# Performance work log

Measured on AMD Instinct MI355X. Metric: run time of the kernel, lower is better.

Reference implementation:

```python
import jax, jax.numpy as jnp
import numpy as np

EMBED_DIM = 1024
N_HEADS = 16
HEAD_SIZE = EMBED_DIM // N_HEADS
SCALE = HEAD_SIZE ** -0.5


def setup_inputs() -> dict:
    key = jax.random.key(0)
    ks = jax.random.split(key, 11)
    B, Tq, Tk, C = 4, 1024, 1024, EMBED_DIM
    std = 0.02
    return {
        "q": jax.random.normal(ks[0], (B, Tq, C), jnp.float32),
        "k": jax.random.normal(ks[1], (B, Tk, C), jnp.float32),
        "v": jax.random.normal(ks[2], (B, Tk, C), jnp.float32),
        "Wq": jax.random.normal(ks[3], (C, C), jnp.float32) * std,
        "bq": jnp.zeros((C,), jnp.float32),
        "Wk": jax.random.normal(ks[4], (C, C), jnp.float32) * std,
        "bk": jnp.zeros((C,), jnp.float32),
        "Wv": jax.random.normal(ks[5], (C, C), jnp.float32) * std,
        "bv": jnp.zeros((C,), jnp.float32),
        "Wo": jax.random.normal(ks[6], (C, C), jnp.float32) * std,
        "bo": jnp.zeros((C,), jnp.float32),
    }


def reference(q, k, v, Wq, bq, Wk, bk, Wv, bv, Wo, bo):
    b, t, c = q.shape
    # linear projections (torch Linear: x @ W.T + b)
    qp = q @ Wq.T + bq            # [b, tq, c]
    kp = k @ Wk.T + bk            # [b, tk, c]
    vp = v @ Wv.T + bv            # [b, tk, c]
    # split heads: [b, h, t, d]
    qh = qp.reshape(b, t, N_HEADS, HEAD_SIZE).transpose(0, 2, 1, 3)
    kh = kp.reshape(b, kp.shape[1], N_HEADS, HEAD_SIZE).transpose(0, 2, 1, 3)
    vh = vp.reshape(b, vp.shape[1], N_HEADS, HEAD_SIZE).transpose(0, 2, 1, 3)
    # scaled dot-product attention
    scores = jnp.einsum('bhqd,bhkd->bhqk', qh, kh) * SCALE
    weights = jax.nn.softmax(scores, axis=-1)
    attn = jnp.einsum('bhqk,bhkd->bhqd', weights, vh)
    attn = attn.transpose(0, 2, 1, 3).reshape(b, t, c)
    out = attn @ Wo.T + bo
    return out
```

## Files before the change

kernel.cpp:

```cpp
#include <hip/hip_runtime.h>
#include <stdint.h>

typedef unsigned short u16;
typedef unsigned int   u32;
typedef __bf16 bf16;
typedef bf16  bf16x2 __attribute__((ext_vector_type(2)));
typedef bf16  bf16x8 __attribute__((ext_vector_type(8)));
typedef float f32x4  __attribute__((ext_vector_type(4)));

#define AS1 __attribute__((address_space(1)))
#define AS3 __attribute__((address_space(3)))


__device__ __forceinline__ u32 pk2(float lo, float hi) {
  bf16x2 t;
  t[0] = (bf16)lo;
  t[1] = (bf16)hi;
  return __builtin_bit_cast(u32, t);
}

__device__ __forceinline__ u16 b1(float f) {
  bf16 t = (bf16)f;
  return __builtin_bit_cast(u16, t);
}

__device__ __forceinline__ void gload_lds16(const void* src, void* dst) {
  __builtin_amdgcn_global_load_lds((const AS1 void*)src, (AS3 void*)dst, 16, 0, 0);
}

__device__ __forceinline__ bf16x8 fragS(const char* lds, int row, int kbyte) {
  return *(const bf16x8*)(lds + row * 128 + (kbyte ^ ((row & 7) << 4)));
}


__global__ __launch_bounds__(256) void cvt_w(
    const float* wq, const float* wk, const float* wv, const float* wo,
    u16* wqb, u16* wkb, u16* wvb, u16* wob)
{
  const float* src; u16* dst;
  switch (blockIdx.y) {
    case 0: src = wq; dst = wqb; break;
    case 1: src = wk; dst = wkb; break;
    case 2: src = wv; dst = wvb; break;
    default: src = wo; dst = wob; break;
  }
  const int n4 = 262144;
  int stride = gridDim.x * blockDim.x;
  for (int i = blockIdx.x * blockDim.x + threadIdx.x; i < n4; i += stride) {
    float4 f = ((const float4*)src)[i];
    uint2 o;
    o.x = pk2(f.x, f.y);
    o.y = pk2(f.z, f.w);
    ((uint2*)dst)[i] = o;
  }
}


template<int NC>
__device__ __forceinline__ void stageSw(const u16* gtile, char* lds, int tid)
{
  int w = tid >> 6, lane = tid & 63;
  int rr = lane >> 3;
  int cb = (lane & 7) << 4;
  #pragma unroll
  for (int i = 0; i < NC; ++i) {
    int c = i * 4 + w;
    int r = c * 8 + rr;
    gload_lds16((const char*)(gtile + r * 1024) + (cb ^ (rr << 4)), lds + c * 1024);
  }
}

__device__ __forceinline__ void loadA64(const float* gA, int tid,
                                        float4* pa, float4* pb)
{
  int r0 = tid >> 3, c8 = (tid & 7) << 3;
  #pragma unroll
  for (int i = 0; i < 2; ++i) {
    const float* p = gA + (i * 32 + r0) * 1024 + c8;
    pa[i] = *(const float4*)p;
    pb[i] = *(const float4*)(p + 4);
  }
}

__device__ __forceinline__ void writeA64(char* lds, int tid,
                                         const float4* pa, const float4* pb)
{
  int r0 = tid >> 3, cb = (tid & 7) << 4;
  #pragma unroll
  for (int i = 0; i < 2; ++i) {
    int r = i * 32 + r0;
    uint4 o;
    o.x = pk2(pa[i].x, pa[i].y);
    o.y = pk2(pa[i].z, pa[i].w);
    o.z = pk2(pb[i].x, pb[i].y);
    o.w = pk2(pb[i].z, pb[i].w);
    *(uint4*)(lds + r * 128 + (cb ^ ((r & 7) << 4))) = o;
  }
}

__device__ __forceinline__ void mfma_64x128(const char* As, const char* Bs,
                                            f32x4 acc[2][4], int lane,
                                            int wr, int wc)
{
  int g = lane >> 4;
  #pragma unroll
  for (int ks = 0; ks < 2; ++ks) {
    int kb = ks * 64 + (g << 4);
    bf16x8 af[2], bfr[4];
    #pragma unroll
    for (int m = 0; m < 2; ++m) af[m]  = fragS(As, wr * 32 + m * 16 + (lane & 15), kb);
    #pragma unroll
    for (int n = 0; n < 4; ++n) bfr[n] = fragS(Bs, wc * 64 + n * 16 + (lane & 15), kb);
    #pragma unroll
    for (int m = 0; m < 2; ++m)
      #pragma unroll
      for (int n = 0; n < 4; ++n)
        acc[m][n] = __builtin_amdgcn_mfma_f32_16x16x32_bf16(af[m], bfr[n], acc[m][n], 0, 0, 0);
  }
}


__global__ __launch_bounds__(256, 4) void proj_gemm(
    const float* qf, const float* kf, const float* vf,
    const u16* wqb, const u16* wkb, const u16* wvb,
    const float* bq, const float* bk, const float* bv,
    u16* qh, u16* kh, u16* vt)
{
  __shared__ alignas(16) char As[8192];
  __shared__ alignas(16) char Bs[16384];
  int tid = threadIdx.x;
  int bi = blockIdx.x & 63, bj = blockIdx.x >> 6;
  int z = blockIdx.z;
  const float* A = (z == 0) ? qf : (z == 1) ? kf : vf;
  const u16* W = (z == 0) ? wqb : (z == 1) ? wkb : wvb;
  const float* bias = (z == 0) ? bq : (z == 1) ? bk : bv;
  u16* dst = (z == 0) ? qh : (z == 1) ? kh : vt;

  int lane = tid & 63;
  int wr = (tid >> 7) & 1, wc = (tid >> 6) & 1;

  float4 pa[2], pb[2];
  loadA64(A + bi * 65536, tid, pa, pb);

  f32x4 acc[2][4] = {};
  for (int kt = 0; kt < 16; ++kt) {
    writeA64(As, tid, pa, pb);
    stageSw<4>(W + bj * 131072 + kt * 64, Bs, tid);
    if (kt < 15)
      loadA64(A + bi * 65536 + (kt + 1) * 64, tid, pa, pb);
    __syncthreads();
    mfma_64x128(As, Bs, acc, lane, wr, wc);
    __syncthreads();
  }

  int rbase = bi * 64 + wr * 32 + ((lane >> 4) << 2);
  int cbase = bj * 128 + wc * 64;
  #pragma unroll
  for (int n = 0; n < 4; ++n) {
    int col = cbase + n * 16 + (lane & 15);
    float bsv = bias[col];
    int h = col >> 6, d = col & 63;
    #pragma unroll
    for (int m = 0; m < 2; ++m) {
      #pragma unroll
      for (int r = 0; r < 4; ++r) {
        int R = rbase + m * 16 + r;
        int b = R >> 10, t = R & 1023;
        u16 val = b1(acc[m][n][r] + bsv);
        if (z < 2) dst[(((b * 16 + h) * 1024 + t) << 6) + d] = val;
        else       dst[(((b * 16 + h) * 64 + d) << 10) + t] = val;
      }
    }
  }
}


__global__ __launch_bounds__(256, 4) void out_gemm(
    const u16* attn, const u16* wob, const float* bo, float* out)
{
  __shared__ alignas(16) char As[8192];
  __shared__ alignas(16) char Bs[16384];
  int tid = threadIdx.x;
  int bi = blockIdx.x & 63, bj = blockIdx.x >> 6;

  int lane = tid & 63;
  int wr = (tid >> 7) & 1, wc = (tid >> 6) & 1;
  f32x4 acc[2][4] = {};
  for (int kt = 0; kt < 16; ++kt) {
    stageSw<2>(attn + bi * 65536  + kt * 64, As, tid);
    stageSw<4>(wob  + bj * 131072 + kt * 64, Bs, tid);
    __syncthreads();
    mfma_64x128(As, Bs, acc, lane, wr, wc);
    __syncthreads();
  }

  int rbase = bi * 64 + wr * 32 + ((lane >> 4) << 2);
  int cbase = bj * 128 + wc * 64;
  #pragma unroll
  for (int n = 0; n < 4; ++n) {
    int col = cbase + n * 16 + (lane & 15);
    float bsv = bo[col];
    #pragma unroll
    for (int m = 0; m < 2; ++m) {
      #pragma unroll
      for (int r = 0; r < 4; ++r) {
        int R = rbase + m * 16 + r;
        out[R * 1024 + col] = acc[m][n][r] + bsv;
      }
    }
  }
}


__global__ __launch_bounds__(256, 2) void attn_fwd(
    const u16* qh, const u16* kh, const u16* vt, u16* attnb)
{
  __shared__ alignas(16) u16 Ks[64 * 72];
  __shared__ alignas(16) u16 Vs[64 * 72];
  __shared__ alignas(16) u16 Pl[4][16 * 72];

  const float SC = 0.125f;
  const float RTHR = 64.0f;

  int tid = threadIdx.x, lane = tid & 63, w = tid >> 6;
  int g = lane >> 4;
  int q0 = blockIdx.x << 6;
  int bh = blockIdx.y;
  const u16* qbase = qh + bh * 65536;
  const u16* kbase = kh + bh * 65536;
  const u16* vbase = vt + bh * 65536;

  bf16x8 qf[2];
  {
    int qrow = q0 + w * 16 + (lane & 15);
    const u16* p = qbase + qrow * 64 + (g << 3);
    qf[0] = *(const bf16x8*)p;
    qf[1] = *(const bf16x8*)(p + 32);
  }

  f32x4 ot[4] = {};
  float m_r = -3.0e38f, l_r = 0.f;

  int sr = tid >> 2;
  int sj = (tid & 3) << 4;
  u16* pw = Pl[w];
  int prow = (lane & 15) * 72;

  for (int kv0 = 0; kv0 < 1024; kv0 += 64) {
    {
      const u16* ksrc = kbase + (kv0 + sr) * 64 + sj;
      const u16* vsrc = vbase + sr * 1024 + kv0 + sj;
      *(bf16x8*)(Ks + sr * 72 + sj)     = *(const bf16x8*)ksrc;
      *(bf16x8*)(Ks + sr * 72 + sj + 8) = *(const bf16x8*)(ksrc + 8);
      *(bf16x8*)(Vs + sr * 72 + sj)     = *(const bf16x8*)vsrc;
      *(bf16x8*)(Vs + sr * 72 + sj + 8) = *(const bf16x8*)(vsrc + 8);
    }
    __syncthreads();

    f32x4 sc[4] = {};
    #pragma unroll
    for (int ks = 0; ks < 2; ++ks) {
      #pragma unroll
      for (int m = 0; m < 4; ++m) {
        bf16x8 kf = *(const bf16x8*)(Ks + (m * 16 + (lane & 15)) * 72 + ks * 32 + g * 8);
        sc[m] = __builtin_amdgcn_mfma_f32_16x16x32_bf16(kf, qf[ks], sc[m], 0, 0, 0);
      }
    }

    float vmax = -3.0e38f;
    #pragma unroll
    for (int m = 0; m < 4; ++m)
      #pragma unroll
      for (int r = 0; r < 4; ++r)
        vmax = fmaxf(vmax, sc[m][r]);
    vmax = fmaxf(vmax, __shfl_xor(vmax, 16, 64));
    vmax = fmaxf(vmax, __shfl_xor(vmax, 32, 64));

    if (!__all(vmax - m_r <= RTHR)) {
      float mnew = fmaxf(m_r, vmax);
      float fac = __expf((m_r - mnew) * SC);
      l_r *= fac;
      #pragma unroll
      for (int dm = 0; dm < 4; ++dm) ot[dm] *= fac;
      m_r = mnew;
    }
    float nm = -m_r * SC;

    float psum = 0.f;
    u32 pp[4][2];
    #pragma unroll
    for (int m = 0; m < 4; ++m) {
      float p0 = __expf(fmaf(sc[m][0], SC, nm));
      float p1 = __expf(fmaf(sc[m][1], SC, nm));
      float p2 = __expf(fmaf(sc[m][2], SC, nm));
      float p3 = __expf(fmaf(sc[m][3], SC, nm));
      psum += (p0 + p1) + (p2 + p3);
      pp[m][0] = pk2(p0, p1);
      pp[m][1] = pk2(p2, p3);
    }
    psum += __shfl_xor(psum, 16, 64);
    psum += __shfl_xor(psum, 32, 64);
    l_r += psum;

    #pragma unroll
    for (int m = 0; m < 4; ++m) {
      u32* d = (u32*)(pw + prow + m * 16 + (g << 2));
      d[0] = pp[m][0];
      d[1] = pp[m][1];
    }

    #pragma unroll
    for (int ks = 0; ks < 2; ++ks) {
      bf16x8 pf = *(const bf16x8*)(pw + prow + ks * 32 + g * 8);
      #pragma unroll
      for (int dm = 0; dm < 4; ++dm) {
        bf16x8 vf = *(const bf16x8*)(Vs + (dm * 16 + (lane & 15)) * 72 + ks * 32 + g * 8);
        ot[dm] = __builtin_amdgcn_mfma_f32_16x16x32_bf16(vf, pf, ot[dm], 0, 0, 0);
      }
    }
    __syncthreads();
  }

  float inv = 1.0f / l_r;
  int b = bh >> 4, h = bh & 15;
  int tok = (b << 10) + q0 + w * 16 + (lane & 15);
  u16* obase = attnb + tok * 1024 + h * 64;
  #pragma unroll
  for (int dm = 0; dm < 4; ++dm) {
    int d0 = dm * 16 + (g << 2);
    u32* d = (u32*)(obase + d0);
    d[0] = pk2(ot[dm][0] * inv, ot[dm][1] * inv);
    d[1] = pk2(ot[dm][2] * inv, ot[dm][3] * inv);
  }
}


extern "C" void kernel_launch(void* const* d_in, const int* in_sizes, int n_in,
                              void* d_out, int out_size, void* d_ws, size_t ws_size,
                              hipStream_t stream)
{
  const float* q  = (const float*)d_in[0];
  const float* k  = (const float*)d_in[1];
  const float* v  = (const float*)d_in[2];
  const float* Wq = (const float*)d_in[3];
  const float* bq = (const float*)d_in[4];
  const float* Wk = (const float*)d_in[5];
  const float* bk = (const float*)d_in[6];
  const float* Wv = (const float*)d_in[7];
  const float* bv = (const float*)d_in[8];
  const float* Wo = (const float*)d_in[9];
  const float* bo = (const float*)d_in[10];
  float* out = (float*)d_out;

  u16* ws  = (u16*)d_ws;
  u16* wqb = ws;
  u16* wkb = wqb + (1u << 20);
  u16* wvb = wkb + (1u << 20);
  u16* wob = wvb + (1u << 20);
  u16* qhb = wob + (1u << 20);
  u16* khb = qhb + (4u << 20);
  u16* vtb = khb + (4u << 20);
  u16* atb = vtb + (4u << 20);

  cvt_w<<<dim3(256, 4, 1), 256, 0, stream>>>(Wq, Wk, Wv, Wo, wqb, wkb, wvb, wob);
  proj_gemm<<<dim3(512, 1, 3), 256, 0, stream>>>(q, k, v, wqb, wkb, wvb,
                                                 bq, bk, bv, qhb, khb, vtb);
  attn_fwd<<<dim3(16, 64, 1), 256, 0, stream>>>(qhb, khb, vtb, atb);
  out_gemm<<<dim3(512, 1, 1), 256, 0, stream>>>(atb, wob, bo, out);
}
```

Measured before the change: 223.5 us.

## Double-buffer GEMM shared tiles and register-prefetch K/V in attention

The projection and output GEMMs now use two LDS buffers, staging tile kt+1 while the MFMAs run on tile kt, which removes one barrier per iteration. Occupancy hints drop from 4 to 3 blocks to make room for the doubled shared memory. The attention kernel prefetches the next K/V tile into registers after the barrier, so the global load latency overlaps with compute. The cost is more LDS and register pressure and possibly lower occupancy.

New measurement: 220.5 us. Within noise of the previous version (-1.3%).

```diff
diff --git a/kernel.cpp b/kernel.cpp
--- a/kernel.cpp
+++ b/kernel.cpp
@@ -120,14 +120,14 @@
 }
 
 
-__global__ __launch_bounds__(256, 4) void proj_gemm(
+__global__ __launch_bounds__(256, 3) void proj_gemm(
     const float* qf, const float* kf, const float* vf,
     const u16* wqb, const u16* wkb, const u16* wvb,
     const float* bq, const float* bk, const float* bv,
     u16* qh, u16* kh, u16* vt)
 {
-  __shared__ alignas(16) char As[8192];
-  __shared__ alignas(16) char Bs[16384];
+  __shared__ alignas(16) char As[2][8192];
+  __shared__ alignas(16) char Bs[2][16384];
   int tid = threadIdx.x;
   int bi = blockIdx.x & 63, bj = blockIdx.x >> 6;
   int z = blockIdx.z;
@@ -141,16 +141,23 @@
 
   float4 pa[2], pb[2];
   loadA64(A + bi * 65536, tid, pa, pb);
+  stageSw<4>(W + bj * 131072, Bs[0], tid);
+  writeA64(As[0], tid, pa, pb);
+  loadA64(A + bi * 65536 + 64, tid, pa, pb);
+  __syncthreads();
 
   f32x4 acc[2][4] = {};
+  int cur = 0;
   for (int kt = 0; kt < 16; ++kt) {
-    writeA64(As, tid, pa, pb);
-    stageSw<4>(W + bj * 131072 + kt * 64, Bs, tid);
-    if (kt < 15)
-      loadA64(A + bi * 65536 + (kt + 1) * 64, tid, pa, pb);
+    if (kt < 15) {
+      stageSw<4>(W + bj * 131072 + (kt + 1) * 64, Bs[cur ^ 1], tid);
+      writeA64(As[cur ^ 1], tid, pa, pb);
+      if (kt < 14)
+        loadA64(A + bi * 65536 + (kt + 2) * 64, tid, pa, pb);
+    }
+    mfma_64x128(As[cur], Bs[cur], acc, lane, wr, wc);
     __syncthreads();
-    mfma_64x128(As, Bs, acc, lane, wr, wc);
-    __syncthreads();
+    cur ^= 1;
   }
 
   int rbase = bi * 64 + wr * 32 + ((lane >> 4) << 2);
@@ -175,23 +182,31 @@
 }
 
 
-__global__ __launch_bounds__(256, 4) void out_gemm(
+__global__ __launch_bounds__(256, 3) void out_gemm(
     const u16* attn, const u16* wob, const float* bo, float* out)
 {
-  __shared__ alignas(16) char As[8192];
-  __shared__ alignas(16) char Bs[16384];
+  __shared__ alignas(16) char As[2][8192];
+  __shared__ alignas(16) char Bs[2][16384];
   int tid = threadIdx.x;
   int bi = blockIdx.x & 63, bj = blockIdx.x >> 6;
 
   int lane = tid & 63;
   int wr = (tid >> 7) & 1, wc = (tid >> 6) & 1;
+
+  stageSw<2>(attn + bi * 65536, As[0], tid);
+  stageSw<4>(wob + bj * 131072, Bs[0], tid);
+  __syncthreads();
+
   f32x4 acc[2][4] = {};
+  int cur = 0;
   for (int kt = 0; kt < 16; ++kt) {
-    stageSw<2>(attn + bi * 65536  + kt * 64, As, tid);
-    stageSw<4>(wob  + bj * 131072 + kt * 64, Bs, tid);
+    if (kt < 15) {
+      stageSw<2>(attn + bi * 65536  + (kt + 1) * 64, As[cur ^ 1], tid);
+      stageSw<4>(wob  + bj * 131072 + (kt + 1) * 64, Bs[cur ^ 1], tid);
+    }
+    mfma_64x128(As[cur], Bs[cur], acc, lane, wr, wc);
     __syncthreads();
-    mfma_64x128(As, Bs, acc, lane, wr, wc);
-    __syncthreads();
+    cur ^= 1;
   }
 
   int rbase = bi * 64 + wr * 32 + ((lane >> 4) << 2);
@@ -246,16 +261,30 @@
   u16* pw = Pl[w];
   int prow = (lane & 15) * 72;
 
+  const u16* ksrc0 = kbase + sr * 64 + sj;
+  const u16* vsrc0 = vbase + sr * 1024 + sj;
+
+  bf16x8 kr0, kr1, vr0, vr1;
+  kr0 = *(const bf16x8*)(ksrc0);
+  kr1 = *(const bf16x8*)(ksrc0 + 8);
+  vr0 = *(const bf16x8*)(vsrc0);
+  vr1 = *(const bf16x8*)(vsrc0 + 8);
+
   for (int kv0 = 0; kv0 < 1024; kv0 += 64) {
-    {
-      const u16* ksrc = kbase + (kv0 + sr) * 64 + sj;
-      const u16* vsrc = vbase + sr * 1024 + kv0 + sj;
-      *(bf16x8*)(Ks + sr * 72 + sj)     = *(const bf16x8*)ksrc;
-      *(bf16x8*)(Ks + sr * 72 + sj + 8) = *(const bf16x8*)(ksrc + 8);
-      *(bf16x8*)(Vs + sr * 72 + sj)     = *(const bf16x8*)vsrc;
-      *(bf16x8*)(Vs + sr * 72 + sj + 8) = *(const bf16x8*)(vsrc + 8);
-    }
+    *(bf16x8*)(Ks + sr * 72 + sj)     = kr0;
+    *(bf16x8*)(Ks + sr * 72 + sj + 8) = kr1;
+    *(bf16x8*)(Vs + sr * 72 + sj)     = vr0;
+    *(bf16x8*)(Vs + sr * 72 + sj + 8) = vr1;
     __syncthreads();
+
+    if (kv0 < 960) {
+      const u16* kn = ksrc0 + (kv0 + 64) * 64;
+      const u16* vn = vsrc0 + (kv0 + 64);
+      kr0 = *(const bf16x8*)(kn);
+      kr1 = *(const bf16x8*)(kn + 8);
+      vr0 = *(const bf16x8*)(vn);
+      vr1 = *(const bf16x8*)(vn + 8);
+    }
 
     f32x4 sc[4] = {};
     #pragma unroll
```
